# Optimization experiments

Measured on AMD Instinct MI355X. Metric: run time of the kernel, lower is better.

The kernel has to match this reference:

```python
import jax, jax.numpy as jnp
import numpy as np

H = 1024      # hidden_size
I = 2048      # intermediate_size
E = 32        # num_routed_experts
B, S = 4, 2048


def setup_inputs() -> dict:
    key = jax.random.key(0)
    ks = jax.random.split(key, 8)
    scale = 0.02
    inp = {
        "hidden_states": jax.random.normal(ks[0], (B, S, H), dtype=jnp.float32),
        # router gate: stored [H, E] so logits = x @ gate_w
        "gate_w": jax.random.normal(ks[1], (H, E), dtype=jnp.float32) * scale,
        # shared SwiGLU (num_shared_experts=1), weights stored [in, out]
        "shared_gate_w": jax.random.normal(ks[2], (H, I), dtype=jnp.float32) * scale,
        "shared_up_w": jax.random.normal(ks[3], (H, I), dtype=jnp.float32) * scale,
        "shared_down_w": jax.random.normal(ks[4], (I, H), dtype=jnp.float32) * scale,
        # routed grouped SwiGLU, weights stored [E, in, out] (matches GroupedLinear)
        "routed_gate_w": jax.random.normal(ks[5], (E, H, I), dtype=jnp.float32) * scale,
        "routed_up_w": jax.random.normal(ks[6], (E, H, I), dtype=jnp.float32) * scale,
        "routed_down_w": jax.random.normal(ks[7], (E, I, H), dtype=jnp.float32) * scale,
    }
    return inp


def _grouped_mm(a, w, group_sizes):
    # a: [T, in], w: [E, in, out], group_sizes: [E] int32 -> [T, out]
    return jax.lax.ragged_dot(a, w, group_sizes)


def _swiglu(x, gw, uw, dw):
    return (jax.nn.silu(x @ gw) * (x @ uw)) @ dw


def reference(hidden_states, gate_w, shared_gate_w, shared_up_w, shared_down_w,
              routed_gate_w, routed_up_w, routed_down_w):
    b, s, h = hidden_states.shape
    x = hidden_states.reshape(-1, h)                      # [T, H]

    # ---- shared expert ----
    shared_out = _swiglu(x, shared_gate_w, shared_up_w, shared_down_w)

    # ---- router: top-1 ----
    logits = x @ gate_w                                   # [T, E]
    topk_ids = jnp.argmax(logits, axis=-1)                # [T]
    topk_val = jnp.max(logits, axis=-1)                   # [T]
    scores = jax.nn.sigmoid(topk_val)[:, None]            # [T, 1]
    xs = x * scores                                       # scale tokens by router score

    # ---- dispatch: sort tokens by expert id ----
    tokens_per_expert = jnp.zeros((E,), jnp.int32).at[topk_ids].add(1)
    order = jnp.argsort(topk_ids)                         # token ids sorted by expert
    sorted_x = xs[order]                                  # [T, H]

    # ---- grouped SwiGLU experts ----
    g = _grouped_mm(sorted_x, routed_gate_w, tokens_per_expert)   # [T, I]
    u = _grouped_mm(sorted_x, routed_up_w, tokens_per_expert)     # [T, I]
    d = _grouped_mm(jax.nn.silu(g) * u, routed_down_w, tokens_per_expert)  # [T, H]

    # ---- combine: unsort back to token order ----
    inv = jnp.argsort(order)
    routed_out = d[inv]

    return (shared_out + routed_out).reshape(b, s, h)
```

## Files before the change

kernel.cpp:

```cpp
#include <hip/hip_runtime.h>
#include <stdint.h>
#include <stddef.h>

#define TOK 8192
#define H 1024
#define IDIM 2048
#define NE 32
#define BM 128
#define BK 64
#define MAX_TILES 96

typedef __attribute__((ext_vector_type(8))) short short8;
typedef __attribute__((ext_vector_type(4))) float f32x4;
typedef __attribute__((ext_vector_type(4))) float float4v;
typedef __attribute__((ext_vector_type(4))) unsigned int uint4v;


__device__ __forceinline__ unsigned short f2bf(float x) {
  unsigned u = __builtin_bit_cast(unsigned, x);
  u += 0x7fffu + ((u >> 16) & 1u);
  return (unsigned short)(u >> 16);
}

__device__ __forceinline__ unsigned cvtpk(float lo, float hi) {
  unsigned r;
  asm("v_cvt_pk_bf16_f32 %0, %1, %2" : "=v"(r) : "v"(lo), "v"(hi));
  return r;
}

__device__ __forceinline__ void gll16(const void* g, void* l) {
  __builtin_amdgcn_global_load_lds(
      (const __attribute__((address_space(1))) unsigned int*)g,
      (__attribute__((address_space(3))) unsigned int*)l, 16, 0, 0);
}

__device__ __forceinline__ f32x4 mfma16(short8 a, short8 b, f32x4 c) {
  return __builtin_amdgcn_mfma_f32_16x16x32_bf16(a, b, c, 0, 0, 0);
}


__global__ __launch_bounds__(256) void tconv_kernel(
    const float* __restrict__ src0, unsigned short* __restrict__ dst0,
    int K, int N)
{
  __shared__ float t[64][65];
  const size_t mat = (size_t)K * N;
  const float* src = src0 + (size_t)blockIdx.z * mat;
  unsigned short* dst = dst0 + (size_t)blockIdx.z * mat;
  const int k0 = blockIdx.x * 64, n0 = blockIdx.y * 64;
  const int tid = threadIdx.x;
  {
    const int r = tid >> 4;
    const int c = (tid & 15) * 4;
    #pragma unroll
    for (int i = 0; i < 4; ++i) {
      float4v v = *(const float4v*)(src + (size_t)(k0 + r + i * 16) * N + (n0 + c));
      t[r + i * 16][c + 0] = v[0];
      t[r + i * 16][c + 1] = v[1];
      t[r + i * 16][c + 2] = v[2];
      t[r + i * 16][c + 3] = v[3];
    }
  }
  __syncthreads();
  {
    const int n = tid >> 2;
    const int kc = (tid & 3) * 16;
    uint4v o0, o1;
    #pragma unroll
    for (int q = 0; q < 4; ++q) {
      o0[q] = cvtpk(t[kc + 2 * q][n],     t[kc + 2 * q + 1][n]);
      o1[q] = cvtpk(t[kc + 8 + 2 * q][n], t[kc + 8 + 2 * q + 1][n]);
    }
    unsigned short* dp = dst + (size_t)(n0 + n) * K + (k0 + kc);
    *(uint4v*)dp = o0;
    *(uint4v*)(dp + 8) = o1;
  }
}


__global__ __launch_bounds__(256) void router_kernel(
    const float* __restrict__ x, const float* __restrict__ gw,
    unsigned short* __restrict__ xbf, unsigned short* __restrict__ xsbf,
    int* __restrict__ expert_id, int* __restrict__ counts)
{
  __shared__ float xl[8 * H];
  __shared__ float plog[8][8][NE];
  __shared__ float sscore[8];
  const int tid = threadIdx.x;
  const long t0 = (long)blockIdx.x * 8;

  const float4v* src = (const float4v*)(x + t0 * H);
  float4v* dst = (float4v*)xl;
  #pragma unroll
  for (int i = 0; i < 8; ++i) dst[tid + i * 256] = src[tid + i * 256];
  __syncthreads();

  {
    const int e = tid & 31, c = tid >> 5;
    float acc[8] = {0, 0, 0, 0, 0, 0, 0, 0};
    const float* gp = gw + (c * 128) * NE + e;
    for (int h = 0; h < 128; ++h) {
      float g = gp[h * NE];
      const float* xr = xl + (c * 128 + h);
      #pragma unroll
      for (int tk = 0; tk < 8; ++tk) acc[tk] += xr[tk * H] * g;
    }
    #pragma unroll
    for (int tk = 0; tk < 8; ++tk) plog[c][tk][e] = acc[tk];
  }
  __syncthreads();
  {
    const int e = tid & 31, tok = tid >> 5;
    float lg = 0.f;
    #pragma unroll
    for (int c = 0; c < 8; ++c) lg += plog[c][tok][e];
    float m = lg; int be = e;
    #pragma unroll
    for (int mask = 16; mask >= 1; mask >>= 1) {
      float om = __shfl_xor(m, mask);
      int   oe = __shfl_xor(be, mask);
      if (om > m || (om == m && oe < be)) { m = om; be = oe; }
    }
    if (e == 0) {
      sscore[tok] = 1.f / (1.f + __expf(-m));
      expert_id[t0 + tok] = be;
      atomicAdd(&counts[be], 1);
    }
  }
  __syncthreads();
  {
    const float sc = sscore[tid >> 5];
    const int base = (tid >> 5) * H + (tid & 31) * 32;
    #pragma unroll
    for (int i = 0; i < 4; ++i) {
      uint4v vx, vs;
      #pragma unroll
      for (int q = 0; q < 4; ++q) {
        const float a = xl[base + i * 8 + 2 * q];
        const float b = xl[base + i * 8 + 2 * q + 1];
        vx[q] = cvtpk(a, b);
        vs[q] = cvtpk(a * sc, b * sc);
      }
      *(uint4v*)(xbf  + t0 * H + base + i * 8) = vx;
      *(uint4v*)(xsbf + t0 * H + base + i * 8) = vs;
    }
  }
}


__global__ void scan_kernel(const int* __restrict__ counts, int* __restrict__ offsets,
                            int* __restrict__ cursor, int* __restrict__ tile_e,
                            int* __restrict__ tile_p, int* __restrict__ n_tiles)
{
  if (threadIdx.x != 0) return;
  int off = 0, nt = 0;
  for (int e = 0; e < NE; ++e) {
    offsets[e] = off; cursor[e] = off;
    int cc = counts[e];
    for (int k = 0; k < cc; k += BM) { tile_e[nt] = e; tile_p[nt] = off + k; ++nt; }
    off += cc;
  }
  offsets[NE] = off;
  n_tiles[0] = nt;
}


__global__ __launch_bounds__(256) void perm_kernel(
    const int* __restrict__ expert_id, int* __restrict__ cursor, int* __restrict__ perm)
{
  int t = blockIdx.x * 256 + threadIdx.x;
  int e = expert_id[t];
  int pos = atomicAdd(&cursor[e], 1);
  perm[pos] = t;
}


template<bool ROUTED>
__global__ __launch_bounds__(256, 2) void gu_kernel(
    const unsigned short* __restrict__ A,
    const unsigned short* __restrict__ GT,
    const unsigned short* __restrict__ UT,
    unsigned short* __restrict__ act,
    const int* __restrict__ perm, const int* __restrict__ tile_e,
    const int* __restrict__ tile_p, const int* __restrict__ offsets,
    const int* __restrict__ n_tiles)
{
  __shared__ short Al[BM * BK];
  __shared__ short Gl[128 * BK];
  __shared__ short Ul[128 * BK];

  const int tid = threadIdx.x;
  const int wave = tid >> 6, lane = tid & 63;
  const int wm = wave >> 1, wn = wave & 1;

  int row0, row_end;
  const unsigned short *Gt, *Ut;
  if constexpr (ROUTED) {
    if ((int)blockIdx.x >= *n_tiles) return;
    const int e = tile_e[blockIdx.x];
    row0 = tile_p[blockIdx.x];
    row_end = offsets[e + 1];
    Gt = GT + (size_t)e * H * IDIM;
    Ut = UT + (size_t)e * H * IDIM;
  } else {
    row0 = blockIdx.x * BM; row_end = row0 + BM;
    Gt = GT; Ut = UT;
  }
  const int n0 = blockIdx.y * 128;

  const unsigned short *asrc[4], *gsrc[4], *usrc[4];
  int soff[4];
  #pragma unroll
  for (int i = 0; i < 4; ++i) {
    const int r = wave * 32 + i * 8 + (lane >> 3);
    int p = row0 + r;
    if (ROUTED && p >= row_end) p = row0;
    int arow = p;
    if constexpr (ROUTED) arow = perm[p];
    const int cb = ((lane & 7) * 16) ^ ((r & 7) << 4);
    asrc[i] = A  + (size_t)arow * H + (cb >> 1);
    gsrc[i] = Gt + (size_t)(n0 + r) * H + (cb >> 1);
    usrc[i] = Ut + (size_t)(n0 + r) * H + (cb >> 1);
    soff[i] = (wave * 32 + i * 8) * BK;
  }

  f32x4 accg[4][4] = {};
  f32x4 accu[4][4] = {};

  #pragma unroll 1
  for (int kt = 0; kt < H / BK; ++kt) {
    __syncthreads();
    #pragma unroll
    for (int i = 0; i < 4; ++i) gll16(asrc[i] + kt * BK, Al + soff[i]);
    #pragma unroll
    for (int i = 0; i < 4; ++i) gll16(gsrc[i] + kt * BK, Gl + soff[i]);
    #pragma unroll
    for (int i = 0; i < 4; ++i) gll16(usrc[i] + kt * BK, Ul + soff[i]);
    __syncthreads();

    #pragma unroll
    for (int kk = 0; kk < 2; ++kk) {
      short8 af[4];
      #pragma unroll
      for (int m = 0; m < 4; ++m) {
        const int r = wm * 64 + m * 16 + (lane & 15);
        const int cb = (kk * 64 + ((lane >> 4) * 16)) ^ ((r & 7) << 4);
        af[m] = *(const short8*)((const char*)Al + r * 128 + cb);
      }
      #pragma unroll
      for (int nf = 0; nf < 4; ++nf) {
        const int n = wn * 64 + nf * 16 + (lane & 15);
        const int cb = (kk * 64 + ((lane >> 4) * 16)) ^ ((n & 7) << 4);
        short8 bg = *(const short8*)((const char*)Gl + n * 128 + cb);
        short8 bu = *(const short8*)((const char*)Ul + n * 128 + cb);
        #pragma unroll
        for (int m = 0; m < 4; ++m) {
          accg[m][nf] = mfma16(af[m], bg, accg[m][nf]);
          accu[m][nf] = mfma16(af[m], bu, accu[m][nf]);
        }
      }
    }
  }

  #pragma unroll
  for (int m = 0; m < 4; ++m)
    #pragma unroll
    for (int nf = 0; nf < 4; ++nf) {
      const int col = n0 + wn * 64 + nf * 16 + (lane & 15);
      #pragma unroll
      for (int j = 0; j < 4; ++j) {
        const int row = row0 + wm * 64 + m * 16 + ((lane >> 4) * 4) + j;
        if (ROUTED && row >= row_end) continue;
        const float g = accg[m][nf][j];
        const float u = accu[m][nf][j];
        const float v = (g / (1.f + __expf(-g))) * u;
        act[(size_t)row * IDIM + col] = f2bf(v);
      }
    }
}


template<bool ROUTED>
__global__ __launch_bounds__(256, 4) void dn_kernel(
    const unsigned short* __restrict__ A,
    const unsigned short* __restrict__ DT,
    float* __restrict__ out,
    const int* __restrict__ perm, const int* __restrict__ tile_e,
    const int* __restrict__ tile_p, const int* __restrict__ offsets,
    const int* __restrict__ n_tiles)
{
  __shared__ short Al[BM * BK];
  __shared__ short Dl[128 * BK];

  const int tid = threadIdx.x;
  const int wave = tid >> 6, lane = tid & 63;
  const int wm = wave >> 1, wn = wave & 1;

  int row0, row_end;
  const unsigned short* Dt;
  if constexpr (ROUTED) {
    if ((int)blockIdx.x >= *n_tiles) return;
    const int e = tile_e[blockIdx.x];
    row0 = tile_p[blockIdx.x];
    row_end = offsets[e + 1];
    Dt = DT + (size_t)e * H * IDIM;
  } else {
    row0 = blockIdx.x * BM; row_end = row0 + BM;
    Dt = DT;
  }
  const int n0 = blockIdx.y * 128;

  const unsigned short *asrc[4], *dsrc[4];
  int soff[4];
  #pragma unroll
  for (int i = 0; i < 4; ++i) {
    const int r = wave * 32 + i * 8 + (lane >> 3);
    int p = row0 + r;
    if (ROUTED && p >= row_end) p = row0;
    const int cb = ((lane & 7) * 16) ^ ((r & 7) << 4);
    asrc[i] = A  + (size_t)p * IDIM + (cb >> 1);
    dsrc[i] = Dt + (size_t)(n0 + r) * IDIM + (cb >> 1);
    soff[i] = (wave * 32 + i * 8) * BK;
  }

  f32x4 acc[4][4] = {};

  #pragma unroll 1
  for (int kt = 0; kt < IDIM / BK; ++kt) {
    __syncthreads();
    #pragma unroll
    for (int i = 0; i < 4; ++i) gll16(asrc[i] + kt * BK, Al + soff[i]);
    #pragma unroll
    for (int i = 0; i < 4; ++i) gll16(dsrc[i] + kt * BK, Dl + soff[i]);
    __syncthreads();

    #pragma unroll
    for (int kk = 0; kk < 2; ++kk) {
      short8 af[4];
      #pragma unroll
      for (int m = 0; m < 4; ++m) {
        const int r = wm * 64 + m * 16 + (lane & 15);
        const int cb = (kk * 64 + ((lane >> 4) * 16)) ^ ((r & 7) << 4);
        af[m] = *(const short8*)((const char*)Al + r * 128 + cb);
      }
      #pragma unroll
      for (int nf = 0; nf < 4; ++nf) {
        const int n = wn * 64 + nf * 16 + (lane & 15);
        const int cb = (kk * 64 + ((lane >> 4) * 16)) ^ ((n & 7) << 4);
        short8 bd = *(const short8*)((const char*)Dl + n * 128 + cb);
        #pragma unroll
        for (int m = 0; m < 4; ++m) acc[m][nf] = mfma16(af[m], bd, acc[m][nf]);
      }
    }
  }

  #pragma unroll
  for (int m = 0; m < 4; ++m)
    #pragma unroll
    for (int nf = 0; nf < 4; ++nf) {
      const int col = n0 + wn * 64 + nf * 16 + (lane & 15);
      #pragma unroll
      for (int j = 0; j < 4; ++j) {
        const int row = row0 + wm * 64 + m * 16 + ((lane >> 4) * 4) + j;
        const float v = acc[m][nf][j];
        if constexpr (ROUTED) {
          if (row < row_end) {
            const int t = perm[row];
            out[(size_t)t * H + col] += v;
          }
        } else {
          out[(size_t)row * H + col] = v;
        }
      }
    }
}


extern "C" void kernel_launch(void* const* d_in, const int* in_sizes, int n_in,
                              void* d_out, int out_size, void* d_ws, size_t ws_size,
                              hipStream_t stream) {
  (void)in_sizes; (void)n_in; (void)out_size; (void)ws_size;
  const float* x      = (const float*)d_in[0];
  const float* gate_w = (const float*)d_in[1];
  const float* sgw    = (const float*)d_in[2];
  const float* suw    = (const float*)d_in[3];
  const float* sdw    = (const float*)d_in[4];
  const float* rgw    = (const float*)d_in[5];
  const float* ruw    = (const float*)d_in[6];
  const float* rdw    = (const float*)d_in[7];
  float* out = (float*)d_out;

  char* ws = (char*)d_ws;
  unsigned short* xbf  = (unsigned short*)(ws + 0);
  unsigned short* xsbf = (unsigned short*)(ws + 16777216);
  unsigned short* act  = (unsigned short*)(ws + 33554432);
  int* perm      = (int*)(ws + 67108864);
  int* expert_id = (int*)(ws + 67141632);
  int* counts    = (int*)(ws + 67174400);
  int* offsets   = (int*)(ws + 67174528);
  int* cursor    = (int*)(ws + 67174784);
  int* tile_e    = (int*)(ws + 67174912);
  int* tile_p    = (int*)(ws + 67175424);
  int* n_tiles   = (int*)(ws + 67175936);
  unsigned short* rgwT = (unsigned short*)(ws + 68157440);
  unsigned short* ruwT = (unsigned short*)(ws + 202375168);
  unsigned short* rdwT = (unsigned short*)(ws + 336592896);
  unsigned short* sgwT = (unsigned short*)(ws + 470810624);
  unsigned short* suwT = (unsigned short*)(ws + 475004928);
  unsigned short* sdwT = (unsigned short*)(ws + 479199232);

  hipMemsetAsync(counts, 0, NE * sizeof(int), stream);

  tconv_kernel<<<dim3(H / 64, IDIM / 64, NE), 256, 0, stream>>>(rgw, rgwT, H, IDIM);
  tconv_kernel<<<dim3(H / 64, IDIM / 64, NE), 256, 0, stream>>>(ruw, ruwT, H, IDIM);
  tconv_kernel<<<dim3(IDIM / 64, H / 64, NE), 256, 0, stream>>>(rdw, rdwT, IDIM, H);
  tconv_kernel<<<dim3(H / 64, IDIM / 64, 1), 256, 0, stream>>>(sgw, sgwT, H, IDIM);
  tconv_kernel<<<dim3(H / 64, IDIM / 64, 1), 256, 0, stream>>>(suw, suwT, H, IDIM);
  tconv_kernel<<<dim3(IDIM / 64, H / 64, 1), 256, 0, stream>>>(sdw, sdwT, IDIM, H);

  router_kernel<<<TOK / 8, 256, 0, stream>>>(x, gate_w, xbf, xsbf, expert_id, counts);
  scan_kernel<<<1, 64, 0, stream>>>(counts, offsets, cursor, tile_e, tile_p, n_tiles);
  perm_kernel<<<TOK / 256, 256, 0, stream>>>(expert_id, cursor, perm);

  gu_kernel<false><<<dim3(TOK / BM, IDIM / 128), 256, 0, stream>>>(
      xbf, sgwT, suwT, act, perm, tile_e, tile_p, offsets, n_tiles);
  dn_kernel<false><<<dim3(TOK / BM, H / 128), 256, 0, stream>>>(
      act, sdwT, out, perm, tile_e, tile_p, offsets, n_tiles);

  gu_kernel<true><<<dim3(MAX_TILES, IDIM / 128), 256, 0, stream>>>(
      xsbf, rgwT, ruwT, act, perm, tile_e, tile_p, offsets, n_tiles);
  dn_kernel<true><<<dim3(MAX_TILES, H / 128), 256, 0, stream>>>(
      act, rdwT, out, perm, tile_e, tile_p, offsets, n_tiles);
}
```

Before: 647.0 us.

## Merge shared and routed expert GEMMs into single launches with atomic combine

```diff
diff --git a/kernel.cpp b/kernel.cpp
--- a/kernel.cpp
+++ b/kernel.cpp
@@ -175,12 +175,12 @@
 }
 
 
-template<bool ROUTED>
 __global__ __launch_bounds__(256, 2) void gu_kernel(
-    const unsigned short* __restrict__ A,
-    const unsigned short* __restrict__ GT,
-    const unsigned short* __restrict__ UT,
-    unsigned short* __restrict__ act,
+    const unsigned short* __restrict__ xbf,
+    const unsigned short* __restrict__ xsbf,
+    const unsigned short* __restrict__ SG, const unsigned short* __restrict__ SU,
+    const unsigned short* __restrict__ RG, const unsigned short* __restrict__ RU,
+    unsigned short* __restrict__ act_sh, unsigned short* __restrict__ act_rt,
     const int* __restrict__ perm, const int* __restrict__ tile_e,
     const int* __restrict__ tile_p, const int* __restrict__ offsets,
     const int* __restrict__ n_tiles)
@@ -193,18 +193,23 @@
   const int wave = tid >> 6, lane = tid & 63;
   const int wm = wave >> 1, wn = wave & 1;
 
+  const bool routed = (int)blockIdx.x >= (TOK / BM);
   int row0, row_end;
-  const unsigned short *Gt, *Ut;
-  if constexpr (ROUTED) {
-    if ((int)blockIdx.x >= *n_tiles) return;
-    const int e = tile_e[blockIdx.x];
-    row0 = tile_p[blockIdx.x];
+  const unsigned short *Gt, *Ut, *A;
+  unsigned short* act;
+  if (routed) {
+    const int tx = (int)blockIdx.x - TOK / BM;
+    if (tx >= *n_tiles) return;
+    const int e = tile_e[tx];
+    row0 = tile_p[tx];
     row_end = offsets[e + 1];
-    Gt = GT + (size_t)e * H * IDIM;
-    Ut = UT + (size_t)e * H * IDIM;
+    Gt = RG + (size_t)e * H * IDIM;
+    Ut = RU + (size_t)e * H * IDIM;
+    A = xsbf; act = act_rt;
   } else {
     row0 = blockIdx.x * BM; row_end = row0 + BM;
-    Gt = GT; Ut = UT;
+    Gt = SG; Ut = SU;
+    A = xbf; act = act_sh;
   }
   const int n0 = blockIdx.y * 128;
 
@@ -214,9 +219,8 @@
   for (int i = 0; i < 4; ++i) {
     const int r = wave * 32 + i * 8 + (lane >> 3);
     int p = row0 + r;
-    if (ROUTED && p >= row_end) p = row0;
-    int arow = p;
-    if constexpr (ROUTED) arow = perm[p];
+    if (routed && p >= row_end) p = row0;
+    const int arow = routed ? perm[p] : p;
     const int cb = ((lane & 7) * 16) ^ ((r & 7) << 4);
     asrc[i] = A  + (size_t)arow * H + (cb >> 1);
     gsrc[i] = Gt + (size_t)(n0 + r) * H + (cb >> 1);
@@ -270,7 +274,7 @@
       #pragma unroll
       for (int j = 0; j < 4; ++j) {
         const int row = row0 + wm * 64 + m * 16 + ((lane >> 4) * 4) + j;
-        if (ROUTED && row >= row_end) continue;
+        if (routed && row >= row_end) continue;
         const float g = accg[m][nf][j];
         const float u = accu[m][nf][j];
         const float v = (g / (1.f + __expf(-g))) * u;
@@ -280,10 +284,10 @@
 }
 
 
-template<bool ROUTED>
 __global__ __launch_bounds__(256, 4) void dn_kernel(
-    const unsigned short* __restrict__ A,
-    const unsigned short* __restrict__ DT,
+    const unsigned short* __restrict__ act_sh,
+    const unsigned short* __restrict__ act_rt,
+    const unsigned short* __restrict__ SD, const unsigned short* __restrict__ RD,
     float* __restrict__ out,
     const int* __restrict__ perm, const int* __restrict__ tile_e,
     const int* __restrict__ tile_p, const int* __restrict__ offsets,
@@ -296,17 +300,21 @@
   const int wave = tid >> 6, lane = tid & 63;
   const int wm = wave >> 1, wn = wave & 1;
 
+  const bool routed = (int)blockIdx.x >= (TOK / BM);
   int row0, row_end;
-  const unsigned short* Dt;
-  if constexpr (ROUTED) {
-    if ((int)blockIdx.x >= *n_tiles) return;
-    const int e = tile_e[blockIdx.x];
-    row0 = tile_p[blockIdx.x];
+  const unsigned short *Dt, *A;
+  if (routed) {
+    const int tx = (int)blockIdx.x - TOK / BM;
+    if (tx >= *n_tiles) return;
+    const int e = tile_e[tx];
+    row0 = tile_p[tx];
     row_end = offsets[e + 1];
-    Dt = DT + (size_t)e * H * IDIM;
+    Dt = RD + (size_t)e * H * IDIM;
+    A = act_rt;
   } else {
     row0 = blockIdx.x * BM; row_end = row0 + BM;
-    Dt = DT;
+    Dt = SD;
+    A = act_sh;
   }
   const int n0 = blockIdx.y * 128;
 
@@ -316,7 +324,7 @@
   for (int i = 0; i < 4; ++i) {
     const int r = wave * 32 + i * 8 + (lane >> 3);
     int p = row0 + r;
-    if (ROUTED && p >= row_end) p = row0;
+    if (routed && p >= row_end) p = row0;
     const int cb = ((lane & 7) * 16) ^ ((r & 7) << 4);
     asrc[i] = A  + (size_t)p * IDIM + (cb >> 1);
     dsrc[i] = Dt + (size_t)(n0 + r) * IDIM + (cb >> 1);
@@ -362,15 +370,10 @@
       #pragma unroll
       for (int j = 0; j < 4; ++j) {
         const int row = row0 + wm * 64 + m * 16 + ((lane >> 4) * 4) + j;
+        if (routed && row >= row_end) continue;
         const float v = acc[m][nf][j];
-        if constexpr (ROUTED) {
-          if (row < row_end) {
-            const int t = perm[row];
-            out[(size_t)t * H + col] += v;
-          }
-        } else {
-          out[(size_t)row * H + col] = v;
-        }
+        const int t = routed ? perm[row] : row;
+        atomicAdd(&out[(size_t)t * H + col], v);
       }
     }
 }
@@ -391,9 +394,9 @@
   float* out = (float*)d_out;
 
   char* ws = (char*)d_ws;
-  unsigned short* xbf  = (unsigned short*)(ws + 0);
-  unsigned short* xsbf = (unsigned short*)(ws + 16777216);
-  unsigned short* act  = (unsigned short*)(ws + 33554432);
+  unsigned short* xbf    = (unsigned short*)(ws + 0);
+  unsigned short* xsbf   = (unsigned short*)(ws + 16777216);
+  unsigned short* act_sh = (unsigned short*)(ws + 33554432);
   int* perm      = (int*)(ws + 67108864);
   int* expert_id = (int*)(ws + 67141632);
   int* counts    = (int*)(ws + 67174400);
@@ -402,14 +405,16 @@
   int* tile_e    = (int*)(ws + 67174912);
   int* tile_p    = (int*)(ws + 67175424);
   int* n_tiles   = (int*)(ws + 67175936);
-  unsigned short* rgwT = (unsigned short*)(ws + 68157440);
-  unsigned short* ruwT = (unsigned short*)(ws + 202375168);
-  unsigned short* rdwT = (unsigned short*)(ws + 336592896);
-  unsigned short* sgwT = (unsigned short*)(ws + 470810624);
-  unsigned short* suwT = (unsigned short*)(ws + 475004928);
-  unsigned short* sdwT = (unsigned short*)(ws + 479199232);
+  unsigned short* rgwT   = (unsigned short*)(ws + 68157440);
+  unsigned short* ruwT   = (unsigned short*)(ws + 202375168);
+  unsigned short* rdwT   = (unsigned short*)(ws + 336592896);
+  unsigned short* sgwT   = (unsigned short*)(ws + 470810624);
+  unsigned short* suwT   = (unsigned short*)(ws + 475004928);
+  unsigned short* sdwT   = (unsigned short*)(ws + 479199232);
+  unsigned short* act_rt = (unsigned short*)(ws + 483393536);
 
   hipMemsetAsync(counts, 0, NE * sizeof(int), stream);
+  hipMemsetAsync(out, 0, (size_t)TOK * H * sizeof(float), stream);
 
   tconv_kernel<<<dim3(H / 64, IDIM / 64, NE), 256, 0, stream>>>(rgw, rgwT, H, IDIM);
   tconv_kernel<<<dim3(H / 64, IDIM / 64, NE), 256, 0, stream>>>(ruw, ruwT, H, IDIM);
@@ -422,13 +427,11 @@
   scan_kernel<<<1, 64, 0, stream>>>(counts, offsets, cursor, tile_e, tile_p, n_tiles);
   perm_kernel<<<TOK / 256, 256, 0, stream>>>(expert_id, cursor, perm);
 
-  gu_kernel<false><<<dim3(TOK / BM, IDIM / 128), 256, 0, stream>>>(
-      xbf, sgwT, suwT, act, perm, tile_e, tile_p, offsets, n_tiles);
-  dn_kernel<false><<<dim3(TOK / BM, H / 128), 256, 0, stream>>>(
-      act, sdwT, out, perm, tile_e, tile_p, offsets, n_tiles);
-
-  gu_kernel<true><<<dim3(MAX_TILES, IDIM / 128), 256, 0, stream>>>(
-      xsbf, rgwT, ruwT, act, perm, tile_e, tile_p, offsets, n_tiles);
-  dn_kernel<true><<<dim3(MAX_TILES, H / 128), 256, 0, stream>>>(
-      act, rdwT, out, perm, tile_e, tile_p, offsets, n_tiles);
-}
+  gu_kernel<<<dim3(TOK / BM + MAX_TILES, IDIM / 128), 256, 0, stream>>>(
+      xbf, xsbf, sgwT, suwT, rgwT, ruwT, act_sh, act_rt,
+      perm, tile_e, tile_p, offsets, n_tiles);
+
+  dn_kernel<<<dim3(TOK / BM + MAX_TILES, H / 128), 256, 0, stream>>>(
+      act_sh, act_rt, sdwT, rdwT, out,
+      perm, tile_e, tile_p, offsets, n_tiles);
+}
```

New measurement: 692.2 us. 7.0% more time.
